# Performance work log

Hardware: AMD Instinct MI355X
Metric: run time of the kernel (lower is better)

The kernel has to match this reference:

```python
import jax, jax.numpy as jnp
import numpy as np

E, T, D, I, G, K = 8, 1024, 1024, 5632, 128, 2  # experts, tokens, hidden, intermediate, gptq group, topk
RENORMALIZE = True


def setup_inputs() -> dict:
    key = jax.random.key(0)
    ks = jax.random.split(key, 6)
    x = jax.random.normal(ks[0], (T, D), dtype=jnp.float32)
    gating_output = jax.random.normal(ks[1], (T, E), dtype=jnp.float32)
    # int4 GPTQ nibbles stored as int32 in [0, 16)
    w1_q = jax.random.randint(ks[2], (E, D, 2 * I), 0, 16, dtype=jnp.int32)
    w2_q = jax.random.randint(ks[3], (E, I, D), 0, 16, dtype=jnp.int32)
    # per-group scales (group size G along the input/contraction dim)
    w1_scale = jax.random.uniform(ks[4], (E, D // G, 2 * I), dtype=jnp.float32) * 0.02
    w2_scale = jax.random.uniform(ks[5], (E, I // G, D), dtype=jnp.float32) * 0.02
    return {"x": x, "gating_output": gating_output, "w1_q": w1_q, "w2_q": w2_q,
            "w1_scale": w1_scale, "w2_scale": w2_scale}


def _dequant(q, scale, group_size):
    # symmetric GPTQ int4: w = (q - 8) * scale, scale broadcast over its group
    s = jnp.repeat(scale, group_size, axis=1)  # [E, Kdim, N]
    return (q.astype(scale.dtype) - 8.0) * s


def reference(x, gating_output, w1_q, w2_q, w1_scale, w2_scale):
    w1 = _dequant(w1_q, w1_scale, G)  # [E, D, 2I]
    w2 = _dequant(w2_q, w2_scale, G)  # [E, I, D]

    # top-k softmax routing (use_grouped_topk=False path)
    probs = jax.nn.softmax(gating_output, axis=-1)        # [T, E]
    topk_w, topk_i = jax.lax.top_k(probs, K)              # [T, K]
    if RENORMALIZE:
        topk_w = topk_w / jnp.sum(topk_w, axis=-1, keepdims=True)
    # dense combine weights [T, E] (zero where expert not selected)
    cw = jnp.sum(jax.nn.one_hot(topk_i, E, dtype=x.dtype) * topk_w[..., None], axis=1)

    # expert MLPs: silu(x @ Wg) * (x @ Wu) @ Wd
    h = jnp.einsum('td,edn->etn', x, w1)                  # [E, T, 2I]
    gate, up = h[..., :I], h[..., I:]
    act = jax.nn.silu(gate) * up                          # [E, T, I]
    y = jnp.einsum('eti,eid->etd', act, w2)               # [E, T, D]

    out = jnp.einsum('te,etd->td', cw, y)                 # [T, D]
    return out
```

## Files before the change

### kernel.cpp

```cpp
#include <hip/hip_runtime.h>
#include <cstdint>
#include <cstddef>

#define E_ 8
#define T_ 1024
#define D_ 1024
#define I_ 5632
#define TWO_I_ 11264
#define NPAD_MAX 2176
#define NGRP_MAX 136

#define WS_ACTF_B 65536
#define WS_XGF_B  (65536 + 24510464)
#define WS_Y_B    WS_XGF_B
#define WS_CNT   0
#define WS_BASEP 8
#define WS_ESLOT 16
#define WS_TOKW  2064
#define WS_ETOK  4112

typedef __attribute__((ext_vector_type(8))) __bf16 bf16x8;
typedef __attribute__((ext_vector_type(4))) float  f32x4;

__device__ __forceinline__ unsigned f2bf(float f) {
    unsigned u = __float_as_uint(f);
    u += 0x7fffu + ((u >> 16) & 1u);
    return u >> 16;
}
__device__ __forceinline__ unsigned pack2bf(float f0, float f1) {
    unsigned a0 = __float_as_uint(f0); a0 += 0x7fffu + ((a0 >> 16) & 1u);
    unsigned a1 = __float_as_uint(f1); a1 += 0x7fffu + ((a1 >> 16) & 1u);
    return (a0 >> 16) | (a1 & 0xffff0000u);
}

__global__ void routing_kernel(const float* __restrict__ gate,
                               int* cnt, int* basep, int* eslot,
                               float* tokw, int* etok)
{
    int t = threadIdx.x;
    if (t < E_) cnt[t] = 0;
    __syncthreads();
    float g[E_];
#pragma unroll
    for (int e = 0; e < E_; ++e) g[e] = gate[t * E_ + e];
    int i0 = 0; float p0 = g[0];
#pragma unroll
    for (int e = 1; e < E_; ++e) if (g[e] > p0) { p0 = g[e]; i0 = e; }
    int i1 = -1; float p1 = -1e30f;
#pragma unroll
    for (int e = 0; e < E_; ++e) if (e != i0 && g[e] > p1) { p1 = g[e]; i1 = e; }
    float w0 = 1.0f / (1.0f + expf(p1 - p0));
    float w1 = 1.0f - w0;
    int s0 = atomicAdd(&cnt[i0], 1);
    int s1 = atomicAdd(&cnt[i1], 1);
    etok[i0 * T_ + s0] = t;
    etok[i1 * T_ + s1] = t;
    eslot[t * 2 + 0] = i0 * T_ + s0;  tokw[t * 2 + 0] = w0;
    eslot[t * 2 + 1] = i1 * T_ + s1;  tokw[t * 2 + 1] = w1;
    __syncthreads();
    if (t == 0) {
        int r = 0;
#pragma unroll
        for (int e = 0; e < E_; ++e) { basep[e] = r; r += (cnt[e] + 15) & ~15; }
    }
}

__global__ void gather_cast_kernel(const float* __restrict__ x,
                                   const int* __restrict__ cnt,
                                   const int* __restrict__ basep,
                                   const int* __restrict__ etok,
                                   unsigned short* __restrict__ xgf)
{
    int e = blockIdx.x >> 6, g = blockIdx.x & 63;
    int n = cnt[e];
    if (g * 16 >= n) return;
    int tid = threadIdx.x;
    int row = g * 16 + (tid & 15);
    row = min(row, n - 1);
    int tok = etok[e * T_ + row];
    const float* xr = x + (size_t)tok * D_;
    unsigned short* dst = xgf + ((size_t)(basep[e] >> 4) + g) * 16384;
#pragma unroll
    for (int it = 0; it < 8; ++it) {
        int c = it * 16 + (tid >> 4);
        float4 v0 = *(const float4*)(xr + c * 8);
        float4 v1 = *(const float4*)(xr + c * 8 + 4);
        uint4 h;
        h.x = pack2bf(v0.x, v0.y); h.y = pack2bf(v0.z, v0.w);
        h.z = pack2bf(v1.x, v1.y); h.w = pack2bf(v1.z, v1.w);
        *(uint4*)(dst + c * 128 + (tid & 15) * 8) = h;
    }
}

__global__ __launch_bounds__(256, 2) void gemm1_kernel(
    const unsigned short* __restrict__ xgf, const int* __restrict__ w1q,
    const float* __restrict__ w1s, const int* __restrict__ cnt,
    const int* __restrict__ basep, unsigned short* __restrict__ actf)
{
    __shared__ unsigned char blds[2][4096];
    int cg = blockIdx.x % 176, e = blockIdx.x / 176;
    int n = cnt[e];
    if (n <= 0) return;
    int npad = (n + 15) & ~15;
    int pb = basep[e];
    int tid = threadIdx.x, lane = tid & 63, w = tid >> 6;
    int l15 = lane & 15, lq = lane >> 4;
    int colg = w & 1, mh = w >> 1;
    int jcol = cg * 32 + colg * 16 + l15;

    int col64 = tid & 63, kg = tid >> 6;
    int jb = (col64 < 32) ? (cg * 32 + col64) : (I_ + cg * 32 + (col64 - 32));
    const int*   gq  = w1q + ((size_t)e * 1024 + kg * 8) * TWO_I_ + jb;
    const float* sqp = w1s + (size_t)e * 8 * TWO_I_ + jb;
    unsigned swr = (unsigned)(col64 >> 4) * 1024 + (unsigned)(kg * 16 + (col64 & 15)) * 16;
    unsigned srd = (unsigned)colg * 1024 + (unsigned)lane * 16;

    int P0[8], P1[8];
    float sc = 0.f, oc = 0.f;

#define G1_ISSUE(KS, P)                                                     \
    { _Pragma("unroll")                                                     \
      for (int i_ = 0; i_ < 8; ++i_)                                        \
          P[i_] = gq[(size_t)((KS) * 32 + i_) * TWO_I_]; }

#define G1_DEQW(KS, P)                                                      \
    { if (((KS) & 3) == 0) { sc = sqp[(size_t)((KS) >> 2) * TWO_I_];        \
                             oc = -8.f * sc; }                              \
      uint4 fr_;                                                            \
      fr_.x = pack2bf((float)P[0]*sc + oc, (float)P[1]*sc + oc);            \
      fr_.y = pack2bf((float)P[2]*sc + oc, (float)P[3]*sc + oc);            \
      fr_.z = pack2bf((float)P[4]*sc + oc, (float)P[5]*sc + oc);            \
      fr_.w = pack2bf((float)P[6]*sc + oc, (float)P[7]*sc + oc);            \
      *(uint4*)(&blds[(KS) & 1][swr]) = fr_; }

    for (int tb = 0; tb < npad; tb += 320) {
        int aoff[10];
#pragma unroll
        for (int mi = 0; mi < 10; ++mi) {
            int R = tb + mh * 160 + mi * 16;
            R = min(R, npad - 16);
            aoff[mi] = ((pb + R) >> 4) * 32768;
        }
        const char* abase = (const char*)xgf + lq * 256 + l15 * 16;

        f32x4 accg[10], accu[10];
#pragma unroll
        for (int mi = 0; mi < 10; ++mi) {
            accg[mi] = (f32x4){0.f, 0.f, 0.f, 0.f};
            accu[mi] = (f32x4){0.f, 0.f, 0.f, 0.f};
        }
        G1_ISSUE(0, P0);
        G1_ISSUE(1, P1);
        G1_DEQW(0, P0);
        G1_ISSUE(2, P0);
        __syncthreads();

#pragma unroll 2
        for (int ks = 0; ks < 32; ++ks) {
            const char* at = abase + ks * 1024;
            bf16x8 a[10];
#pragma unroll
            for (int mi = 0; mi < 10; ++mi)
                a[mi] = *(const bf16x8*)(at + aoff[mi]);
            bf16x8 bg = *(const bf16x8*)(&blds[ks & 1][srd]);
            bf16x8 bu = *(const bf16x8*)(&blds[ks & 1][srd + 2048]);
            if (ks < 31) {
                if (ks & 1) {
                    G1_DEQW(ks + 1, P0);
                    if (ks < 29) { G1_ISSUE(ks + 3, P0); }
                } else {
                    G1_DEQW(ks + 1, P1);
                    if (ks < 29) { G1_ISSUE(ks + 3, P1); }
                }
            }
#pragma unroll
            for (int mi = 0; mi < 10; ++mi) {
                accg[mi] = __builtin_amdgcn_mfma_f32_16x16x32_bf16(a[mi], bg, accg[mi], 0, 0, 0);
                accu[mi] = __builtin_amdgcn_mfma_f32_16x16x32_bf16(a[mi], bu, accu[mi], 0, 0, 0);
            }
            __syncthreads();
        }
#pragma unroll
        for (int mi = 0; mi < 10; ++mi) {
#pragma unroll
            for (int r = 0; r < 4; ++r) {
                int ml = mh * 160 + mi * 16 + lq * 4 + r;
                int m = tb + ml;
                if (m < npad) {
                    float gv = accg[mi][r], uv = accu[mi][r];
                    float av = gv / (1.f + __expf(-gv)) * uv;
                    int prow = pb + m;
                    size_t o = (size_t)(prow >> 4) * 90112 + (jcol >> 3) * 128
                             + (prow & 15) * 8 + (jcol & 7);
                    actf[o] = (unsigned short)f2bf(av);
                }
            }
        }
    }
#undef G1_ISSUE
#undef G1_DEQW
}

__global__ __launch_bounds__(256, 2) void gemm2_kernel(
    const unsigned short* __restrict__ actf, const int* __restrict__ w2q,
    const float* __restrict__ w2s, const int* __restrict__ cnt,
    const int* __restrict__ basep, float* __restrict__ y)
{
    __shared__ unsigned char blds[2][4096];
    int bid = blockIdx.x;
    int seg = bid & 3, dt = (bid >> 2) & 15, e = bid >> 6;
    int n = cnt[e];
    if (n <= 0) return;
    int npad = (n + 15) & ~15;
    int pb = basep[e];
    int tid = threadIdx.x, lane = tid & 63, w = tid >> 6;
    int l15 = lane & 15, lq = lane >> 4;
    int colg = w & 1, mh = w >> 1;
    int dcol = dt * 64 + colg * 32 + l15;

    int col64 = tid & 63, kg = tid >> 6;
    int colb = dt * 64 + col64;
    const int*   gq  = w2q + ((size_t)e * 5632 + seg * 1408 + kg * 8) * 1024 + colb;
    const float* sqp = w2s + ((size_t)e * 44 + seg * 11) * 1024 + colb;
    unsigned swr = (unsigned)(col64 >> 4) * 1024 + (unsigned)(kg * 16 + (col64 & 15)) * 16;
    unsigned srd = (unsigned)(colg * 2) * 1024 + (unsigned)lane * 16;

    int P0[8], P1[8];
    float sc = 0.f, oc = 0.f;

#define G2_ISSUE(KS, P)                                                     \
    { _Pragma("unroll")                                                     \
      for (int i_ = 0; i_ < 8; ++i_)                                        \
          P[i_] = gq[(size_t)((KS) * 32 + i_) * 1024]; }

#define G2_DEQW(KS, P)                                                      \
    { if (((KS) & 3) == 0) { sc = sqp[(size_t)((KS) >> 2) * 1024];          \
                             oc = -8.f * sc; }                              \
      uint4 fr_;                                                            \
      fr_.x = pack2bf((float)P[0]*sc + oc, (float)P[1]*sc + oc);            \
      fr_.y = pack2bf((float)P[2]*sc + oc, (float)P[3]*sc + oc);            \
      fr_.z = pack2bf((float)P[4]*sc + oc, (float)P[5]*sc + oc);            \
      fr_.w = pack2bf((float)P[6]*sc + oc, (float)P[7]*sc + oc);            \
      *(uint4*)(&blds[(KS) & 1][swr]) = fr_; }

    for (int tb = 0; tb < npad; tb += 320) {
        int aoff[10];
#pragma unroll
        for (int mi = 0; mi < 10; ++mi) {
            int R = tb + mh * 160 + mi * 16;
            R = min(R, npad - 16);
            aoff[mi] = ((pb + R) >> 4) * 180224;
        }
        const char* abase = (const char*)actf + seg * 45056 + lq * 256 + l15 * 16;

        f32x4 acc0[10], acc1[10];
#pragma unroll
        for (int mi = 0; mi < 10; ++mi) {
            acc0[mi] = (f32x4){0.f, 0.f, 0.f, 0.f};
            acc1[mi] = (f32x4){0.f, 0.f, 0.f, 0.f};
        }
        G2_ISSUE(0, P0);
        G2_ISSUE(1, P1);
        G2_DEQW(0, P0);
        G2_ISSUE(2, P0);
        __syncthreads();

#pragma unroll 2
        for (int ks = 0; ks < 44; ++ks) {
            const char* at = abase + ks * 1024;
            bf16x8 a[10];
#pragma unroll
            for (int mi = 0; mi < 10; ++mi)
                a[mi] = *(const bf16x8*)(at + aoff[mi]);
            bf16x8 b0 = *(const bf16x8*)(&blds[ks & 1][srd]);
            bf16x8 b1 = *(const bf16x8*)(&blds[ks & 1][srd + 1024]);
            if (ks < 43) {
                if (ks & 1) {
                    G2_DEQW(ks + 1, P0);
                    if (ks < 41) { G2_ISSUE(ks + 3, P0); }
                } else {
                    G2_DEQW(ks + 1, P1);
                    if (ks < 41) { G2_ISSUE(ks + 3, P1); }
                }
            }
#pragma unroll
            for (int mi = 0; mi < 10; ++mi) {
                acc0[mi] = __builtin_amdgcn_mfma_f32_16x16x32_bf16(a[mi], b0, acc0[mi], 0, 0, 0);
                acc1[mi] = __builtin_amdgcn_mfma_f32_16x16x32_bf16(a[mi], b1, acc1[mi], 0, 0, 0);
            }
            __syncthreads();
        }
#pragma unroll
        for (int mi = 0; mi < 10; ++mi) {
#pragma unroll
            for (int r = 0; r < 4; ++r) {
                int m = tb + mh * 160 + mi * 16 + lq * 4 + r;
                if (m < n) {
                    float* yr = y + (size_t)seg * NPAD_MAX * 1024 + (size_t)(pb + m) * 1024;
                    yr[dcol]      = acc0[mi][r];
                    yr[dcol + 16] = acc1[mi][r];
                }
            }
        }
    }
#undef G2_ISSUE
#undef G2_DEQW
}

__global__ void combine_kernel(const float* __restrict__ y,
                               const int* __restrict__ eslot,
                               const float* __restrict__ tokw,
                               const int* __restrict__ basep,
                               float* __restrict__ out)
{
    int idx = blockIdx.x * blockDim.x + threadIdx.x;
    int t  = idx >> 8;
    int dc = idx & 255;
    int es0 = eslot[t * 2 + 0], es1 = eslot[t * 2 + 1];
    float w0 = tokw[t * 2 + 0], w1 = tokw[t * 2 + 1];
    int p0 = basep[es0 >> 10] + (es0 & 1023);
    int p1 = basep[es1 >> 10] + (es1 & 1023);
    const float4* y4 = (const float4*)y;
    float4 o = (float4){0.f, 0.f, 0.f, 0.f};
#pragma unroll
    for (int seg = 0; seg < 4; ++seg) {
        float4 a = y4[((size_t)seg * NPAD_MAX + p0) * 256 + dc];
        float4 b = y4[((size_t)seg * NPAD_MAX + p1) * 256 + dc];
        o.x += w0 * a.x + w1 * b.x;
        o.y += w0 * a.y + w1 * b.y;
        o.z += w0 * a.z + w1 * b.z;
        o.w += w0 * a.w + w1 * b.w;
    }
    ((float4*)out)[idx] = o;
}

extern "C" void kernel_launch(void* const* d_in, const int* in_sizes, int n_in,
                              void* d_out, int out_size, void* d_ws, size_t ws_size,
                              hipStream_t stream)
{
    const float* x    = (const float*)d_in[0];
    const float* gate = (const float*)d_in[1];
    const int*   w1q  = (const int*)d_in[2];
    const int*   w2q  = (const int*)d_in[3];
    const float* w1s  = (const float*)d_in[4];
    const float* w2s  = (const float*)d_in[5];
    float* out = (float*)d_out;
    int*   wsi = (int*)d_ws;
    float* wsf = (float*)d_ws;

    int*   cnt   = wsi + WS_CNT;
    int*   basep = wsi + WS_BASEP;
    int*   eslot = wsi + WS_ESLOT;
    float* tokw  = wsf + WS_TOKW;
    int*   etok  = wsi + WS_ETOK;
    unsigned short* actf = (unsigned short*)((char*)d_ws + WS_ACTF_B);
    unsigned short* xgf  = (unsigned short*)((char*)d_ws + WS_XGF_B);
    float*          y    = (float*)((char*)d_ws + WS_Y_B);

    routing_kernel<<<1, 1024, 0, stream>>>(gate, cnt, basep, eslot, tokw, etok);
    gather_cast_kernel<<<E_ * 64, 256, 0, stream>>>(x, cnt, basep, etok, xgf);
    gemm1_kernel<<<E_ * 176, 256, 0, stream>>>(xgf, w1q, w1s, cnt, basep, actf);
    gemm2_kernel<<<E_ * 16 * 4, 256, 0, stream>>>(actf, w2q, w2s, cnt, basep, y);
    combine_kernel<<<(T_ * D_ / 4) / 256, 256, 0, stream>>>(y, eslot, tokw, basep, out);
}
```

Measured before the change: 714.0 us.

## Process two k-steps per barrier in GEMM kernels with quad-buffered LDS

Both grouped GEMM kernels now consume two 32-wide k-slices per barrier, using a 4-slot LDS buffer and 16-register prefetch sets. This halves the number of block barriers. It also adds explicit s_waitcnt, sched_barrier and setprio around the MFMA bursts so that loads and dequantisation finish before the matrix work and the MFMAs get issue priority. The cost is higher register pressure from doubled A fragments and prefetch registers, which may cause spills at launch bound 2, plus more LDS per block.

```diff
diff --git a/kernel.cpp b/kernel.cpp
--- a/kernel.cpp
+++ b/kernel.cpp
@@ -97,7 +97,7 @@
     const float* __restrict__ w1s, const int* __restrict__ cnt,
     const int* __restrict__ basep, unsigned short* __restrict__ actf)
 {
-    __shared__ unsigned char blds[2][4096];
+    __shared__ unsigned char blds[16384];
     int cg = blockIdx.x % 176, e = blockIdx.x / 176;
     int n = cnt[e];
     if (n <= 0) return;
@@ -115,23 +115,29 @@
     unsigned swr = (unsigned)(col64 >> 4) * 1024 + (unsigned)(kg * 16 + (col64 & 15)) * 16;
     unsigned srd = (unsigned)colg * 1024 + (unsigned)lane * 16;
 
-    int P0[8], P1[8];
+    int PA[16], PB[16];
     float sc = 0.f, oc = 0.f;
 
-#define G1_ISSUE(KS, P)                                                     \
+#define G1_ISSUE2(T, P)                                                     \
     { _Pragma("unroll")                                                     \
       for (int i_ = 0; i_ < 8; ++i_)                                        \
-          P[i_] = gq[(size_t)((KS) * 32 + i_) * TWO_I_]; }
-
-#define G1_DEQW(KS, P)                                                      \
+          P[i_] = gq[(size_t)((T) * 64 + i_) * TWO_I_];                     \
+      _Pragma("unroll")                                                     \
+      for (int i_ = 0; i_ < 8; ++i_)                                        \
+          P[8 + i_] = gq[(size_t)((T) * 64 + 32 + i_) * TWO_I_]; }
+
+#define G1_DEQW1(KS, P, O)                                                  \
     { if (((KS) & 3) == 0) { sc = sqp[(size_t)((KS) >> 2) * TWO_I_];        \
                              oc = -8.f * sc; }                              \
       uint4 fr_;                                                            \
-      fr_.x = pack2bf((float)P[0]*sc + oc, (float)P[1]*sc + oc);            \
-      fr_.y = pack2bf((float)P[2]*sc + oc, (float)P[3]*sc + oc);            \
-      fr_.z = pack2bf((float)P[4]*sc + oc, (float)P[5]*sc + oc);            \
-      fr_.w = pack2bf((float)P[6]*sc + oc, (float)P[7]*sc + oc);            \
-      *(uint4*)(&blds[(KS) & 1][swr]) = fr_; }
+      fr_.x = pack2bf((float)P[(O)+0]*sc + oc, (float)P[(O)+1]*sc + oc);    \
+      fr_.y = pack2bf((float)P[(O)+2]*sc + oc, (float)P[(O)+3]*sc + oc);    \
+      fr_.z = pack2bf((float)P[(O)+4]*sc + oc, (float)P[(O)+5]*sc + oc);    \
+      fr_.w = pack2bf((float)P[(O)+6]*sc + oc, (float)P[(O)+7]*sc + oc);    \
+      *(uint4*)(&blds[((((KS) >> 1) & 1) * 8192) + (((KS) & 1) * 4096)      \
+                      + swr]) = fr_; }
+
+#define G1_DEQW2(T, P)  { G1_DEQW1((2*(T)), P, 0) G1_DEQW1((2*(T)+1), P, 8) }
 
     for (int tb = 0; tb < npad; tb += 320) {
         int aoff[10];
@@ -149,36 +155,80 @@
             accg[mi] = (f32x4){0.f, 0.f, 0.f, 0.f};
             accu[mi] = (f32x4){0.f, 0.f, 0.f, 0.f};
         }
-        G1_ISSUE(0, P0);
-        G1_ISSUE(1, P1);
-        G1_DEQW(0, P0);
-        G1_ISSUE(2, P0);
-        __syncthreads();
-
-#pragma unroll 2
-        for (int ks = 0; ks < 32; ++ks) {
-            const char* at = abase + ks * 1024;
-            bf16x8 a[10];
-#pragma unroll
-            for (int mi = 0; mi < 10; ++mi)
-                a[mi] = *(const bf16x8*)(at + aoff[mi]);
-            bf16x8 bg = *(const bf16x8*)(&blds[ks & 1][srd]);
-            bf16x8 bu = *(const bf16x8*)(&blds[ks & 1][srd + 2048]);
-            if (ks < 31) {
-                if (ks & 1) {
-                    G1_DEQW(ks + 1, P0);
-                    if (ks < 29) { G1_ISSUE(ks + 3, P0); }
-                } else {
-                    G1_DEQW(ks + 1, P1);
-                    if (ks < 29) { G1_ISSUE(ks + 3, P1); }
-                }
-            }
-#pragma unroll
-            for (int mi = 0; mi < 10; ++mi) {
-                accg[mi] = __builtin_amdgcn_mfma_f32_16x16x32_bf16(a[mi], bg, accg[mi], 0, 0, 0);
-                accu[mi] = __builtin_amdgcn_mfma_f32_16x16x32_bf16(a[mi], bu, accu[mi], 0, 0, 0);
-            }
-            __syncthreads();
+        G1_ISSUE2(0, PA);
+        G1_ISSUE2(1, PB);
+        G1_DEQW2(0, PA);
+        G1_ISSUE2(2, PA);
+        asm volatile("s_waitcnt lgkmcnt(0)" ::: "memory");
+        __builtin_amdgcn_s_barrier();
+        asm volatile("" ::: "memory");
+
+#pragma unroll 1
+        for (int s2 = 0; s2 < 8; ++s2) {
+            {
+                const char* at = abase + (size_t)s2 * 4096;
+                bf16x8 a0[10], a1[10];
+#pragma unroll
+                for (int mi = 0; mi < 10; ++mi)
+                    a0[mi] = *(const bf16x8*)(at + aoff[mi]);
+#pragma unroll
+                for (int mi = 0; mi < 10; ++mi)
+                    a1[mi] = *(const bf16x8*)(at + 1024 + aoff[mi]);
+                bf16x8 bg0 = *(const bf16x8*)(&blds[srd]);
+                bf16x8 bu0 = *(const bf16x8*)(&blds[srd + 2048]);
+                bf16x8 bg1 = *(const bf16x8*)(&blds[4096 + srd]);
+                bf16x8 bu1 = *(const bf16x8*)(&blds[4096 + srd + 2048]);
+                G1_DEQW2(2*s2 + 1, PB);
+                if (s2 < 7) { G1_ISSUE2(2*s2 + 3, PB); }
+                asm volatile("s_waitcnt lgkmcnt(0)" ::: "memory");
+                __builtin_amdgcn_sched_barrier(0);
+                __builtin_amdgcn_s_setprio(1);
+#pragma unroll
+                for (int mi = 0; mi < 10; ++mi) {
+                    accg[mi] = __builtin_amdgcn_mfma_f32_16x16x32_bf16(a0[mi], bg0, accg[mi], 0, 0, 0);
+                    accu[mi] = __builtin_amdgcn_mfma_f32_16x16x32_bf16(a0[mi], bu0, accu[mi], 0, 0, 0);
+                }
+#pragma unroll
+                for (int mi = 0; mi < 10; ++mi) {
+                    accg[mi] = __builtin_amdgcn_mfma_f32_16x16x32_bf16(a1[mi], bg1, accg[mi], 0, 0, 0);
+                    accu[mi] = __builtin_amdgcn_mfma_f32_16x16x32_bf16(a1[mi], bu1, accu[mi], 0, 0, 0);
+                }
+                __builtin_amdgcn_s_setprio(0);
+                __builtin_amdgcn_s_barrier();
+                asm volatile("" ::: "memory");
+            }
+            {
+                const char* at = abase + (size_t)s2 * 4096 + 2048;
+                bf16x8 a0[10], a1[10];
+#pragma unroll
+                for (int mi = 0; mi < 10; ++mi)
+                    a0[mi] = *(const bf16x8*)(at + aoff[mi]);
+#pragma unroll
+                for (int mi = 0; mi < 10; ++mi)
+                    a1[mi] = *(const bf16x8*)(at + 1024 + aoff[mi]);
+                bf16x8 bg0 = *(const bf16x8*)(&blds[8192 + srd]);
+                bf16x8 bu0 = *(const bf16x8*)(&blds[8192 + srd + 2048]);
+                bf16x8 bg1 = *(const bf16x8*)(&blds[12288 + srd]);
+                bf16x8 bu1 = *(const bf16x8*)(&blds[12288 + srd + 2048]);
+                if (s2 < 7) { G1_DEQW2(2*s2 + 2, PA); }
+                if (s2 < 6) { G1_ISSUE2(2*s2 + 4, PA); }
+                asm volatile("s_waitcnt lgkmcnt(0)" ::: "memory");
+                __builtin_amdgcn_sched_barrier(0);
+                __builtin_amdgcn_s_setprio(1);
+#pragma unroll
+                for (int mi = 0; mi < 10; ++mi) {
+                    accg[mi] = __builtin_amdgcn_mfma_f32_16x16x32_bf16(a0[mi], bg0, accg[mi], 0, 0, 0);
+                    accu[mi] = __builtin_amdgcn_mfma_f32_16x16x32_bf16(a0[mi], bu0, accu[mi], 0, 0, 0);
+                }
+#pragma unroll
+                for (int mi = 0; mi < 10; ++mi) {
+                    accg[mi] = __builtin_amdgcn_mfma_f32_16x16x32_bf16(a1[mi], bg1, accg[mi], 0, 0, 0);
+                    accu[mi] = __builtin_amdgcn_mfma_f32_16x16x32_bf16(a1[mi], bu1, accu[mi], 0, 0, 0);
+                }
+                __builtin_amdgcn_s_setprio(0);
+                __builtin_amdgcn_s_barrier();
+                asm volatile("" ::: "memory");
+            }
         }
 #pragma unroll
         for (int mi = 0; mi < 10; ++mi) {
@@ -197,8 +247,9 @@
             }
         }
     }
-#undef G1_ISSUE
-#undef G1_DEQW
+#undef G1_ISSUE2
+#undef G1_DEQW1
+#undef G1_DEQW2
 }
 
 __global__ __launch_bounds__(256, 2) void gemm2_kernel(
@@ -206,7 +257,7 @@
     const float* __restrict__ w2s, const int* __restrict__ cnt,
     const int* __restrict__ basep, float* __restrict__ y)
 {
-    __shared__ unsigned char blds[2][4096];
+    __shared__ unsigned char blds[16384];
     int bid = blockIdx.x;
     int seg = bid & 3, dt = (bid >> 2) & 15, e = bid >> 6;
     int n = cnt[e];
@@ -225,23 +276,29 @@
     unsigned swr = (unsigned)(col64 >> 4) * 1024 + (unsigned)(kg * 16 + (col64 & 15)) * 16;
     unsigned srd = (unsigned)(colg * 2) * 1024 + (unsigned)lane * 16;
 
-    int P0[8], P1[8];
+    int PA[16], PB[16];
     float sc = 0.f, oc = 0.f;
 
-#define G2_ISSUE(KS, P)                                                     \
+#define G2_ISSUE2(T, P)                                                     \
     { _Pragma("unroll")                                                     \
       for (int i_ = 0; i_ < 8; ++i_)                                        \
-          P[i_] = gq[(size_t)((KS) * 32 + i_) * 1024]; }
-
-#define G2_DEQW(KS, P)                                                      \
+          P[i_] = gq[(size_t)((T) * 64 + i_) * 1024];                       \
+      _Pragma("unroll")                                                     \
+      for (int i_ = 0; i_ < 8; ++i_)                                        \
+          P[8 + i_] = gq[(size_t)((T) * 64 + 32 + i_) * 1024]; }
+
+#define G2_DEQW1(KS, P, O)                                                  \
     { if (((KS) & 3) == 0) { sc = sqp[(size_t)((KS) >> 2) * 1024];          \
                              oc = -8.f * sc; }                              \
       uint4 fr_;                                                            \
-      fr_.x = pack2bf((float)P[0]*sc + oc, (float)P[1]*sc + oc);            \
-      fr_.y = pack2bf((float)P[2]*sc + oc, (float)P[3]*sc + oc);            \
-      fr_.z = pack2bf((float)P[4]*sc + oc, (float)P[5]*sc + oc);            \
-      fr_.w = pack2bf((float)P[6]*sc + oc, (float)P[7]*sc + oc);            \
-      *(uint4*)(&blds[(KS) & 1][swr]) = fr_; }
+      fr_.x = pack2bf((float)P[(O)+0]*sc + oc, (float)P[(O)+1]*sc + oc);    \
+      fr_.y = pack2bf((float)P[(O)+2]*sc + oc, (float)P[(O)+3]*sc + oc);    \
+      fr_.z = pack2bf((float)P[(O)+4]*sc + oc, (float)P[(O)+5]*sc + oc);    \
+      fr_.w = pack2bf((float)P[(O)+6]*sc + oc, (float)P[(O)+7]*sc + oc);    \
+      *(uint4*)(&blds[((((KS) >> 1) & 1) * 8192) + (((KS) & 1) * 4096)      \
+                      + swr]) = fr_; }
+
+#define G2_DEQW2(T, P)  { G2_DEQW1((2*(T)), P, 0) G2_DEQW1((2*(T)+1), P, 8) }
 
     for (int tb = 0; tb < npad; tb += 320) {
         int aoff[10];
@@ -259,36 +316,80 @@
             acc0[mi] = (f32x4){0.f, 0.f, 0.f, 0.f};
             acc1[mi] = (f32x4){0.f, 0.f, 0.f, 0.f};
         }
-        G2_ISSUE(0, P0);
-        G2_ISSUE(1, P1);
-        G2_DEQW(0, P0);
-        G2_ISSUE(2, P0);
-        __syncthreads();
-
-#pragma unroll 2
-        for (int ks = 0; ks < 44; ++ks) {
-            const char* at = abase + ks * 1024;
-            bf16x8 a[10];
-#pragma unroll
-            for (int mi = 0; mi < 10; ++mi)
-                a[mi] = *(const bf16x8*)(at + aoff[mi]);
-            bf16x8 b0 = *(const bf16x8*)(&blds[ks & 1][srd]);
-            bf16x8 b1 = *(const bf16x8*)(&blds[ks & 1][srd + 1024]);
-            if (ks < 43) {
-                if (ks & 1) {
-                    G2_DEQW(ks + 1, P0);
-                    if (ks < 41) { G2_ISSUE(ks + 3, P0); }
-                } else {
-                    G2_DEQW(ks + 1, P1);
-                    if (ks < 41) { G2_ISSUE(ks + 3, P1); }
-                }
-            }
-#pragma unroll
-            for (int mi = 0; mi < 10; ++mi) {
-                acc0[mi] = __builtin_amdgcn_mfma_f32_16x16x32_bf16(a[mi], b0, acc0[mi], 0, 0, 0);
-                acc1[mi] = __builtin_amdgcn_mfma_f32_16x16x32_bf16(a[mi], b1, acc1[mi], 0, 0, 0);
-            }
-            __syncthreads();
+        G2_ISSUE2(0, PA);
+        G2_ISSUE2(1, PB);
+        G2_DEQW2(0, PA);
+        G2_ISSUE2(2, PA);
+        asm volatile("s_waitcnt lgkmcnt(0)" ::: "memory");
+        __builtin_amdgcn_s_barrier();
+        asm volatile("" ::: "memory");
+
+#pragma unroll 1
+        for (int s2 = 0; s2 < 11; ++s2) {
+            {
+                const char* at = abase + (size_t)s2 * 4096;
+                bf16x8 a0[10], a1[10];
+#pragma unroll
+                for (int mi = 0; mi < 10; ++mi)
+                    a0[mi] = *(const bf16x8*)(at + aoff[mi]);
+#pragma unroll
+                for (int mi = 0; mi < 10; ++mi)
+                    a1[mi] = *(const bf16x8*)(at + 1024 + aoff[mi]);
+                bf16x8 b00 = *(const bf16x8*)(&blds[srd]);
+                bf16x8 b01 = *(const bf16x8*)(&blds[srd + 1024]);
+                bf16x8 b10 = *(const bf16x8*)(&blds[4096 + srd]);
+                bf16x8 b11 = *(const bf16x8*)(&blds[4096 + srd + 1024]);
+                G2_DEQW2(2*s2 + 1, PB);
+                if (s2 < 10) { G2_ISSUE2(2*s2 + 3, PB); }
+                asm volatile("s_waitcnt lgkmcnt(0)" ::: "memory");
+                __builtin_amdgcn_sched_barrier(0);
+                __builtin_amdgcn_s_setprio(1);
+#pragma unroll
+                for (int mi = 0; mi < 10; ++mi) {
+                    acc0[mi] = __builtin_amdgcn_mfma_f32_16x16x32_bf16(a0[mi], b00, acc0[mi], 0, 0, 0);
+                    acc1[mi] = __builtin_amdgcn_mfma_f32_16x16x32_bf16(a0[mi], b01, acc1[mi], 0, 0, 0);
+                }
+#pragma unroll
+                for (int mi = 0; mi < 10; ++mi) {
+                    acc0[mi] = __builtin_amdgcn_mfma_f32_16x16x32_bf16(a1[mi], b10, acc0[mi], 0, 0, 0);
+                    acc1[mi] = __builtin_amdgcn_mfma_f32_16x16x32_bf16(a1[mi], b11, acc1[mi], 0, 0, 0);
+                }
+                __builtin_amdgcn_s_setprio(0);
+                __builtin_amdgcn_s_barrier();
+                asm volatile("" ::: "memory");
+            }
+            {
+                const char* at = abase + (size_t)s2 * 4096 + 2048;
+                bf16x8 a0[10], a1[10];
+#pragma unroll
+                for (int mi = 0; mi < 10; ++mi)
+                    a0[mi] = *(const bf16x8*)(at + aoff[mi]);
+#pragma unroll
+                for (int mi = 0; mi < 10; ++mi)
+                    a1[mi] = *(const bf16x8*)(at + 1024 + aoff[mi]);
+                bf16x8 b00 = *(const bf16x8*)(&blds[8192 + srd]);
+                bf16x8 b01 = *(const bf16x8*)(&blds[8192 + srd + 1024]);
+                bf16x8 b10 = *(const bf16x8*)(&blds[12288 + srd]);
+                bf16x8 b11 = *(const bf16x8*)(&blds[12288 + srd + 1024]);
+                if (s2 < 10) { G2_DEQW2(2*s2 + 2, PA); }
+                if (s2 < 9)  { G2_ISSUE2(2*s2 + 4, PA); }
+                asm volatile("s_waitcnt lgkmcnt(0)" ::: "memory");
+                __builtin_amdgcn_sched_barrier(0);
+                __builtin_amdgcn_s_setprio(1);
+#pragma unroll
+                for (int mi = 0; mi < 10; ++mi) {
+                    acc0[mi] = __builtin_amdgcn_mfma_f32_16x16x32_bf16(a0[mi], b00, acc0[mi], 0, 0, 0);
+                    acc1[mi] = __builtin_amdgcn_mfma_f32_16x16x32_bf16(a0[mi], b01, acc1[mi], 0, 0, 0);
+                }
+#pragma unroll
+                for (int mi = 0; mi < 10; ++mi) {
+                    acc0[mi] = __builtin_amdgcn_mfma_f32_16x16x32_bf16(a1[mi], b10, acc0[mi], 0, 0, 0);
+                    acc1[mi] = __builtin_amdgcn_mfma_f32_16x16x32_bf16(a1[mi], b11, acc1[mi], 0, 0, 0);
+                }
+                __builtin_amdgcn_s_setprio(0);
+                __builtin_amdgcn_s_barrier();
+                asm volatile("" ::: "memory");
+            }
         }
 #pragma unroll
         for (int mi = 0; mi < 10; ++mi) {
@@ -303,8 +404,9 @@
             }
         }
     }
-#undef G2_ISSUE
-#undef G2_DEQW
+#undef G2_ISSUE2
+#undef G2_DEQW1
+#undef G2_DEQW2
 }
 
 __global__ void combine_kernel(const float* __restrict__ y,
```

Measured after the change: 844.4 us. 1.18x slower.

## Split GEMM tiles across eight waves with four-stage weight prefetch

Applied to the files above, without the earlier changes.

Both dequant-GEMM kernels move from 256 to 512 threads per block. Each wave now owns half as many M-rows (5 instead of 10 MFMA row tiles) and loads 4 instead of 8 k-rows of int4 weights, writing half-width slots into the LDS B tile. The register prefetch ring deepens from two slots to four, with scales loaded per slot. The per-step __syncthreads is replaced by an explicit lgkmcnt wait plus s_barrier, so in-flight global loads are not drained at each barrier. This aims to hide more global-load latency and raise wave-level parallelism. The risk is register pressure under launch_bounds(512,4), which could cause spills or lower real occupancy.

```diff
diff --git a/kernel.cpp b/kernel.cpp
--- a/kernel.cpp
+++ b/kernel.cpp
@@ -92,7 +92,7 @@
     }
 }
 
-__global__ __launch_bounds__(256, 2) void gemm1_kernel(
+__global__ __launch_bounds__(512, 4) void gemm1_kernel(
     const unsigned short* __restrict__ xgf, const int* __restrict__ w1q,
     const float* __restrict__ w1s, const int* __restrict__ cnt,
     const int* __restrict__ basep, unsigned short* __restrict__ actf)
@@ -108,83 +108,87 @@
     int colg = w & 1, mh = w >> 1;
     int jcol = cg * 32 + colg * 16 + l15;
 
-    int col64 = tid & 63, kg = tid >> 6;
+    int col64 = lane, kg = w;
     int jb = (col64 < 32) ? (cg * 32 + col64) : (I_ + cg * 32 + (col64 - 32));
-    const int*   gq  = w1q + ((size_t)e * 1024 + kg * 8) * TWO_I_ + jb;
+    const int*   gq  = w1q + ((size_t)e * 1024 + kg * 4) * TWO_I_ + jb;
     const float* sqp = w1s + (size_t)e * 8 * TWO_I_ + jb;
-    unsigned swr = (unsigned)(col64 >> 4) * 1024 + (unsigned)(kg * 16 + (col64 & 15)) * 16;
+    unsigned swr = (unsigned)(col64 >> 4) * 1024
+                 + (unsigned)((kg >> 1) * 16 + (col64 & 15)) * 16
+                 + (unsigned)(kg & 1) * 8;
     unsigned srd = (unsigned)colg * 1024 + (unsigned)lane * 16;
 
-    int P0[8], P1[8];
-    float sc = 0.f, oc = 0.f;
-
-#define G1_ISSUE(KS, P)                                                     \
+    int P0[4], P1[4], P2[4], P3[4];
+    float S0, S1, S2, S3;
+
+#define G1_ISSUE(S, P, SS)                                                  \
     { _Pragma("unroll")                                                     \
-      for (int i_ = 0; i_ < 8; ++i_)                                        \
-          P[i_] = gq[(size_t)((KS) * 32 + i_) * TWO_I_]; }
-
-#define G1_DEQW(KS, P)                                                      \
-    { if (((KS) & 3) == 0) { sc = sqp[(size_t)((KS) >> 2) * TWO_I_];        \
-                             oc = -8.f * sc; }                              \
-      uint4 fr_;                                                            \
-      fr_.x = pack2bf((float)P[0]*sc + oc, (float)P[1]*sc + oc);            \
-      fr_.y = pack2bf((float)P[2]*sc + oc, (float)P[3]*sc + oc);            \
-      fr_.z = pack2bf((float)P[4]*sc + oc, (float)P[5]*sc + oc);            \
-      fr_.w = pack2bf((float)P[6]*sc + oc, (float)P[7]*sc + oc);            \
-      *(uint4*)(&blds[(KS) & 1][swr]) = fr_; }
+      for (int i_ = 0; i_ < 4; ++i_)                                        \
+          P[i_] = gq[(size_t)((S) * 32 + i_) * TWO_I_];                     \
+      SS = sqp[(size_t)((S) >> 2) * TWO_I_]; }
+
+#define G1_DEQW(S, P, SS)                                                   \
+    { float oc_ = -8.f * SS;                                                \
+      uint2 fr_;                                                            \
+      fr_.x = pack2bf((float)P[0]*SS + oc_, (float)P[1]*SS + oc_);          \
+      fr_.y = pack2bf((float)P[2]*SS + oc_, (float)P[3]*SS + oc_);          \
+      *(uint2*)(&blds[(S) & 1][swr]) = fr_; }
 
     for (int tb = 0; tb < npad; tb += 320) {
-        int aoff[10];
-#pragma unroll
-        for (int mi = 0; mi < 10; ++mi) {
-            int R = tb + mh * 160 + mi * 16;
+        int aoff[5];
+#pragma unroll
+        for (int mi = 0; mi < 5; ++mi) {
+            int R = tb + mh * 80 + mi * 16;
             R = min(R, npad - 16);
             aoff[mi] = ((pb + R) >> 4) * 32768;
         }
         const char* abase = (const char*)xgf + lq * 256 + l15 * 16;
 
-        f32x4 accg[10], accu[10];
-#pragma unroll
-        for (int mi = 0; mi < 10; ++mi) {
+        f32x4 accg[5], accu[5];
+#pragma unroll
+        for (int mi = 0; mi < 5; ++mi) {
             accg[mi] = (f32x4){0.f, 0.f, 0.f, 0.f};
             accu[mi] = (f32x4){0.f, 0.f, 0.f, 0.f};
         }
-        G1_ISSUE(0, P0);
-        G1_ISSUE(1, P1);
-        G1_DEQW(0, P0);
-        G1_ISSUE(2, P0);
-        __syncthreads();
-
-#pragma unroll 2
-        for (int ks = 0; ks < 32; ++ks) {
-            const char* at = abase + ks * 1024;
-            bf16x8 a[10];
-#pragma unroll
-            for (int mi = 0; mi < 10; ++mi)
+        G1_ISSUE(0, P0, S0);
+        G1_ISSUE(1, P1, S1);
+        G1_ISSUE(2, P2, S2);
+        G1_ISSUE(3, P3, S3);
+        G1_DEQW(0, P0, S0);
+        G1_ISSUE(4, P0, S0);
+        asm volatile("s_waitcnt lgkmcnt(0)" ::: "memory");
+        __builtin_amdgcn_s_barrier();
+        asm volatile("" ::: "memory");
+
+#pragma unroll 4
+        for (int s = 0; s < 32; ++s) {
+            const char* at = abase + (size_t)s * 1024;
+            bf16x8 a[5];
+#pragma unroll
+            for (int mi = 0; mi < 5; ++mi)
                 a[mi] = *(const bf16x8*)(at + aoff[mi]);
-            bf16x8 bg = *(const bf16x8*)(&blds[ks & 1][srd]);
-            bf16x8 bu = *(const bf16x8*)(&blds[ks & 1][srd + 2048]);
-            if (ks < 31) {
-                if (ks & 1) {
-                    G1_DEQW(ks + 1, P0);
-                    if (ks < 29) { G1_ISSUE(ks + 3, P0); }
-                } else {
-                    G1_DEQW(ks + 1, P1);
-                    if (ks < 29) { G1_ISSUE(ks + 3, P1); }
-                }
-            }
-#pragma unroll
-            for (int mi = 0; mi < 10; ++mi) {
+            if (s + 1 < 32) {
+                const int sl = (s + 1) & 3;
+                if (sl == 0)      { G1_DEQW(s+1, P0, S0); if (s+5 < 32) { G1_ISSUE(s+5, P0, S0); } }
+                else if (sl == 1) { G1_DEQW(s+1, P1, S1); if (s+5 < 32) { G1_ISSUE(s+5, P1, S1); } }
+                else if (sl == 2) { G1_DEQW(s+1, P2, S2); if (s+5 < 32) { G1_ISSUE(s+5, P2, S2); } }
+                else              { G1_DEQW(s+1, P3, S3); if (s+5 < 32) { G1_ISSUE(s+5, P3, S3); } }
+            }
+            bf16x8 bg = *(const bf16x8*)(&blds[s & 1][srd]);
+            bf16x8 bu = *(const bf16x8*)(&blds[s & 1][srd + 2048]);
+#pragma unroll
+            for (int mi = 0; mi < 5; ++mi) {
                 accg[mi] = __builtin_amdgcn_mfma_f32_16x16x32_bf16(a[mi], bg, accg[mi], 0, 0, 0);
                 accu[mi] = __builtin_amdgcn_mfma_f32_16x16x32_bf16(a[mi], bu, accu[mi], 0, 0, 0);
             }
-            __syncthreads();
-        }
-#pragma unroll
-        for (int mi = 0; mi < 10; ++mi) {
+            asm volatile("s_waitcnt lgkmcnt(0)" ::: "memory");
+            __builtin_amdgcn_s_barrier();
+            asm volatile("" ::: "memory");
+        }
+#pragma unroll
+        for (int mi = 0; mi < 5; ++mi) {
 #pragma unroll
             for (int r = 0; r < 4; ++r) {
-                int ml = mh * 160 + mi * 16 + lq * 4 + r;
+                int ml = mh * 80 + mi * 16 + lq * 4 + r;
                 int m = tb + ml;
                 if (m < npad) {
                     float gv = accg[mi][r], uv = accu[mi][r];
@@ -201,7 +205,7 @@
 #undef G1_DEQW
 }
 
-__global__ __launch_bounds__(256, 2) void gemm2_kernel(
+__global__ __launch_bounds__(512, 4) void gemm2_kernel(
     const unsigned short* __restrict__ actf, const int* __restrict__ w2q,
     const float* __restrict__ w2s, const int* __restrict__ cnt,
     const int* __restrict__ basep, float* __restrict__ y)
@@ -218,83 +222,87 @@
     int colg = w & 1, mh = w >> 1;
     int dcol = dt * 64 + colg * 32 + l15;
 
-    int col64 = tid & 63, kg = tid >> 6;
+    int col64 = lane, kg = w;
     int colb = dt * 64 + col64;
-    const int*   gq  = w2q + ((size_t)e * 5632 + seg * 1408 + kg * 8) * 1024 + colb;
+    const int*   gq  = w2q + ((size_t)e * 5632 + seg * 1408 + kg * 4) * 1024 + colb;
     const float* sqp = w2s + ((size_t)e * 44 + seg * 11) * 1024 + colb;
-    unsigned swr = (unsigned)(col64 >> 4) * 1024 + (unsigned)(kg * 16 + (col64 & 15)) * 16;
-    unsigned srd = (unsigned)(colg * 2) * 1024 + (unsigned)lane * 16;
-
-    int P0[8], P1[8];
-    float sc = 0.f, oc = 0.f;
-
-#define G2_ISSUE(KS, P)                                                     \
+    unsigned swr = (unsigned)(col64 >> 4) * 1024
+                 + (unsigned)((kg >> 1) * 16 + (col64 & 15)) * 16
+                 + (unsigned)(kg & 1) * 8;
+    unsigned srd = (unsigned)colg * 2048 + (unsigned)lane * 16;
+
+    int P0[4], P1[4], P2[4], P3[4];
+    float S0, S1, S2, S3;
+
+#define G2_ISSUE(S, P, SS)                                                  \
     { _Pragma("unroll")                                                     \
-      for (int i_ = 0; i_ < 8; ++i_)                                        \
-          P[i_] = gq[(size_t)((KS) * 32 + i_) * 1024]; }
-
-#define G2_DEQW(KS, P)                                                      \
-    { if (((KS) & 3) == 0) { sc = sqp[(size_t)((KS) >> 2) * 1024];          \
-                             oc = -8.f * sc; }                              \
-      uint4 fr_;                                                            \
-      fr_.x = pack2bf((float)P[0]*sc + oc, (float)P[1]*sc + oc);            \
-      fr_.y = pack2bf((float)P[2]*sc + oc, (float)P[3]*sc + oc);            \
-      fr_.z = pack2bf((float)P[4]*sc + oc, (float)P[5]*sc + oc);            \
-      fr_.w = pack2bf((float)P[6]*sc + oc, (float)P[7]*sc + oc);            \
-      *(uint4*)(&blds[(KS) & 1][swr]) = fr_; }
+      for (int i_ = 0; i_ < 4; ++i_)                                        \
+          P[i_] = gq[(size_t)((S) * 32 + i_) * 1024];                       \
+      SS = sqp[(size_t)((S) >> 2) * 1024]; }
+
+#define G2_DEQW(S, P, SS)                                                   \
+    { float oc_ = -8.f * SS;                                                \
+      uint2 fr_;                                                            \
+      fr_.x = pack2bf((float)P[0]*SS + oc_, (float)P[1]*SS + oc_);          \
+      fr_.y = pack2bf((float)P[2]*SS + oc_, (float)P[3]*SS + oc_);          \
+      *(uint2*)(&blds[(S) & 1][swr]) = fr_; }
 
     for (int tb = 0; tb < npad; tb += 320) {
-        int aoff[10];
-#pragma unroll
-        for (int mi = 0; mi < 10; ++mi) {
-            int R = tb + mh * 160 + mi * 16;
+        int aoff[5];
+#pragma unroll
+        for (int mi = 0; mi < 5; ++mi) {
+            int R = tb + mh * 80 + mi * 16;
             R = min(R, npad - 16);
             aoff[mi] = ((pb + R) >> 4) * 180224;
         }
         const char* abase = (const char*)actf + seg * 45056 + lq * 256 + l15 * 16;
 
-        f32x4 acc0[10], acc1[10];
-#pragma unroll
-        for (int mi = 0; mi < 10; ++mi) {
+        f32x4 acc0[5], acc1[5];
+#pragma unroll
+        for (int mi = 0; mi < 5; ++mi) {
             acc0[mi] = (f32x4){0.f, 0.f, 0.f, 0.f};
             acc1[mi] = (f32x4){0.f, 0.f, 0.f, 0.f};
         }
-        G2_ISSUE(0, P0);
-        G2_ISSUE(1, P1);
-        G2_DEQW(0, P0);
-        G2_ISSUE(2, P0);
-        __syncthreads();
-
-#pragma unroll 2
-        for (int ks = 0; ks < 44; ++ks) {
-            const char* at = abase + ks * 1024;
-            bf16x8 a[10];
-#pragma unroll
-            for (int mi = 0; mi < 10; ++mi)
+        G2_ISSUE(0, P0, S0);
+        G2_ISSUE(1, P1, S1);
+        G2_ISSUE(2, P2, S2);
+        G2_ISSUE(3, P3, S3);
+        G2_DEQW(0, P0, S0);
+        G2_ISSUE(4, P0, S0);
+        asm volatile("s_waitcnt lgkmcnt(0)" ::: "memory");
+        __builtin_amdgcn_s_barrier();
+        asm volatile("" ::: "memory");
+
+#pragma unroll 4
+        for (int s = 0; s < 44; ++s) {
+            const char* at = abase + (size_t)s * 1024;
+            bf16x8 a[5];
+#pragma unroll
+            for (int mi = 0; mi < 5; ++mi)
                 a[mi] = *(const bf16x8*)(at + aoff[mi]);
-            bf16x8 b0 = *(const bf16x8*)(&blds[ks & 1][srd]);
-            bf16x8 b1 = *(const bf16x8*)(&blds[ks & 1][srd + 1024]);
-            if (ks < 43) {
-                if (ks & 1) {
-                    G2_DEQW(ks + 1, P0);
-                    if (ks < 41) { G2_ISSUE(ks + 3, P0); }
-                } else {
-                    G2_DEQW(ks + 1, P1);
-                    if (ks < 41) { G2_ISSUE(ks + 3, P1); }
-                }
-            }
-#pragma unroll
-            for (int mi = 0; mi < 10; ++mi) {
+            if (s + 1 < 44) {
+                const int sl = (s + 1) & 3;
+                if (sl == 0)      { G2_DEQW(s+1, P0, S0); if (s+5 < 44) { G2_ISSUE(s+5, P0, S0); } }
+                else if (sl == 1) { G2_DEQW(s+1, P1, S1); if (s+5 < 44) { G2_ISSUE(s+5, P1, S1); } }
+                else if (sl == 2) { G2_DEQW(s+1, P2, S2); if (s+5 < 44) { G2_ISSUE(s+5, P2, S2); } }
+                else              { G2_DEQW(s+1, P3, S3); if (s+5 < 44) { G2_ISSUE(s+5, P3, S3); } }
+            }
+            bf16x8 b0 = *(const bf16x8*)(&blds[s & 1][srd]);
+            bf16x8 b1 = *(const bf16x8*)(&blds[s & 1][srd + 1024]);
+#pragma unroll
+            for (int mi = 0; mi < 5; ++mi) {
                 acc0[mi] = __builtin_amdgcn_mfma_f32_16x16x32_bf16(a[mi], b0, acc0[mi], 0, 0, 0);
                 acc1[mi] = __builtin_amdgcn_mfma_f32_16x16x32_bf16(a[mi], b1, acc1[mi], 0, 0, 0);
             }
-            __syncthreads();
-        }
-#pragma unroll
-        for (int mi = 0; mi < 10; ++mi) {
+            asm volatile("s_waitcnt lgkmcnt(0)" ::: "memory");
+            __builtin_amdgcn_s_barrier();
+            asm volatile("" ::: "memory");
+        }
+#pragma unroll
+        for (int mi = 0; mi < 5; ++mi) {
 #pragma unroll
             for (int r = 0; r < 4; ++r) {
-                int m = tb + mh * 160 + mi * 16 + lq * 4 + r;
+                int m = tb + mh * 80 + mi * 16 + lq * 4 + r;
                 if (m < n) {
                     float* yr = y + (size_t)seg * NPAD_MAX * 1024 + (size_t)(pb + m) * 1024;
                     yr[dcol]      = acc0[mi][r];
@@ -359,7 +367,7 @@
 
     routing_kernel<<<1, 1024, 0, stream>>>(gate, cnt, basep, eslot, tokw, etok);
     gather_cast_kernel<<<E_ * 64, 256, 0, stream>>>(x, cnt, basep, etok, xgf);
-    gemm1_kernel<<<E_ * 176, 256, 0, stream>>>(xgf, w1q, w1s, cnt, basep, actf);
-    gemm2_kernel<<<E_ * 16 * 4, 256, 0, stream>>>(actf, w2q, w2s, cnt, basep, y);
+    gemm1_kernel<<<E_ * 176, 512, 0, stream>>>(xgf, w1q, w1s, cnt, basep, actf);
+    gemm2_kernel<<<E_ * 16 * 4, 512, 0, stream>>>(actf, w2q, w2s, cnt, basep, y);
     combine_kernel<<<(T_ * D_ / 4) / 256, 256, 0, stream>>>(y, eslot, tokw, basep, out);
 }
```

New measurement: 741.4 us. +3.8%, slower.
